# Optimization experiments

Measured on AMD Instinct MI355X. Metric: run time of the kernel, lower is better.

Reference implementation:

```python
import jax, jax.numpy as jnp
import numpy as np

SPACIAL_SCALE = 1.0 / 32
POOLED = 7  # original uses (pooled_height, pooled_height) for both dims


def setup_inputs() -> dict:
    key = jax.random.key(0)
    k_f, k_b, k_x, k_y = jax.random.split(key, 4)
    N, C, H, W = 4, 256, 64, 64
    R = 256
    img = 2047.0  # image-space extent (stride 32 -> 64 feature cells)
    features = jax.random.normal(k_f, (N, C, H, W), dtype=jnp.float32)
    bidx = jax.random.randint(k_b, (R,), 0, N).astype(jnp.float32)
    xs = jnp.sort(jax.random.uniform(k_x, (R, 2), dtype=jnp.float32) * img, axis=1)
    ys = jnp.sort(jax.random.uniform(k_y, (R, 2), dtype=jnp.float32) * img, axis=1)
    # roi = (batch_idx, x_min, y_min, x_max, y_max)
    rois = jnp.stack([bidx, xs[:, 0], ys[:, 0], xs[:, 1], ys[:, 1]], axis=1)
    return {"features": features, "rois": rois}


def _roi_pool(features, rois):
    N, C, H, W = features.shape
    P = POOLED
    neg = -jnp.inf

    bidx = rois[:, 0].astype(jnp.int32)
    # np.round rounds half-to-even; jnp.round matches
    bbox = jnp.round(rois[:, 1:] * SPACIAL_SCALE).astype(jnp.int32)  # [R,4]
    x0 = jnp.clip(bbox[:, 0], 0, W - 1)
    y0 = jnp.clip(bbox[:, 1], 0, H - 1)
    x1 = jnp.clip(bbox[:, 2], 0, W - 1)
    y1 = jnp.clip(bbox[:, 3], 0, H - 1)
    valid = (x0 < x1) & (y0 < y1)  # [R]

    g = features[bidx]  # [R,C,H,W] gathered per-roi feature maps
    Lh = x1 - x0  # rows (H axis) get the x-range -- quirk of the original slice
    Lw = y1 - y0  # cols (W axis) get the y-range

    idx_h = jnp.arange(H)
    idx_w = jnp.arange(W)

    # adaptive_max_pool2d bins: start=floor(i*L/P), end=ceil((i+1)*L/P)
    # Stage 1: reduce W axis into P column bins -> [R,C,H,P]
    cols = []
    for j in range(P):
        s = y0 + (j * Lw) // P
        e = y0 + ((j + 1) * Lw + P - 1) // P
        m = (idx_w[None, :] >= s[:, None]) & (idx_w[None, :] < e[:, None])  # [R,W]
        cols.append(jnp.max(jnp.where(m[:, None, None, :], g, neg), axis=-1))
    s1 = jnp.stack(cols, axis=-1)  # [R,C,H,P]

    # Stage 2: reduce H axis into P row bins -> [R,C,P,P]
    rows = []
    for i in range(P):
        s = x0 + (i * Lh) // P
        e = x0 + ((i + 1) * Lh + P - 1) // P
        m = (idx_h[None, :] >= s[:, None]) & (idx_h[None, :] < e[:, None])  # [R,H]
        rows.append(jnp.max(jnp.where(m[:, None, :, None], s1, neg), axis=2))
    out = jnp.stack(rows, axis=2)  # [R,C,P,P]

    # degenerate rois stay zero (pooled initialized with torch.zeros)
    return jnp.where(valid[:, None, None, None], out, jnp.zeros((), out.dtype))


def reference(features, rois):
    return _roi_pool(features, rois)
```

## Files before the change

### kernel.cpp

```cpp
#include <hip/hip_runtime.h>
#include <math.h>

#define P 7
#define PP (P * P)
#define C 256
#define H 64
#define W 64
#define S (H * W)
#define R_MAX 1024

#define NCP 25
#define RPAD 257

#define TT 64
#define TPAD 65
__global__ __launch_bounds__(256) void transpose_bucket_kernel(
    const float* __restrict__ in, float* __restrict__ outT,
    const float* __restrict__ rois, int* __restrict__ perm, int R)
{
    __shared__ float tile[TT * TPAD];
    const int b   = blockIdx.z;
    const int s0  = blockIdx.x * TT;
    const int c0  = blockIdx.y * TT;
    const int t   = threadIdx.x;
    const int r16 = t >> 4;
    const int m16 = (t & 15) * 4;

    #pragma unroll
    for (int k = 0; k < 4; ++k) {
        const int cl = r16 + 16 * k;
        const float4 v = *(const float4*)(in + (size_t)(b * C + c0 + cl) * S + s0 + m16);
        tile[cl * TPAD + m16 + 0] = v.x;
        tile[cl * TPAD + m16 + 1] = v.y;
        tile[cl * TPAD + m16 + 2] = v.z;
        tile[cl * TPAD + m16 + 3] = v.w;
    }
    __syncthreads();
    #pragma unroll
    for (int k = 0; k < 4; ++k) {
        const int sl = r16 + 16 * k;
        float4 v;
        v.x = tile[(m16 + 0) * TPAD + sl];
        v.y = tile[(m16 + 1) * TPAD + sl];
        v.z = tile[(m16 + 2) * TPAD + sl];
        v.w = tile[(m16 + 3) * TPAD + sl];
        *(float4*)(outT + (size_t)(b * S + s0 + sl) * C + c0 + m16) = v;
    }

    if (blockIdx.x == 0 && blockIdx.y == 0 && blockIdx.z == 0 && R > 0 && R <= R_MAX) {
        __shared__ int bimg[R_MAX];
        for (int i = t; i < R; i += 256)
            bimg[i] = (int)rois[(size_t)i * 5];
        __syncthreads();
        for (int i = t; i < R; i += 256) {
            const int myb = bimg[i];
            int pos = 0;
            for (int k = 0; k < R; ++k) {
                const int bk = bimg[k];
                pos += (bk < myb) || (bk == myb && k < i);
            }
            perm[pos] = i;
        }
    }
}

__global__ __launch_bounds__(128) void roi_pool_cell_kernel(
    const float* __restrict__ ft,
    const float* __restrict__ rois,
    const int*   __restrict__ perm,
    float* __restrict__ ws2)
{
    const int l   = blockIdx.x;
    const int nwg = gridDim.x;
    const int work  = ((nwg & 7) == 0) ? ((l & 7) * (nwg >> 3) + (l >> 3)) : l;
    const int rslot = work / NCP;
    const int cp    = work % NCP;
    const int cell  = 2 * cp + (threadIdx.x >> 6);
    const int q     = threadIdx.x & 63;

    if (cell >= PP) return;

    const int r = perm[rslot];
    const float* roi = rois + (size_t)r * 5;
    const int b = (int)roi[0];
    int x0 = (int)rintf(roi[1] * 0.03125f);
    int y0 = (int)rintf(roi[2] * 0.03125f);
    int x1 = (int)rintf(roi[3] * 0.03125f);
    int y1 = (int)rintf(roi[4] * 0.03125f);
    x0 = min(max(x0, 0), W - 1);
    y0 = min(max(y0, 0), H - 1);
    x1 = min(max(x1, 0), W - 1);
    y1 = min(max(y1, 0), H - 1);

    float4* o = (float4*)(ws2 + ((size_t)rslot * PP + cell) * C) + q;

    if (!((x0 < x1) && (y0 < y1))) {
        *o = make_float4(0.0f, 0.0f, 0.0f, 0.0f);
        return;
    }

    const int Lh = x1 - x0;
    const int Lw = y1 - y0;
    const int i  = cell / P;
    const int j  = cell - P * i;

    const int hs = x0 + (i * Lh) / P;
    const int he = x0 + ((i + 1) * Lh + (P - 1)) / P;
    const int ws = y0 + (j * Lw) / P;
    const int we = y0 + ((j + 1) * Lw + (P - 1)) / P;
    const int bh = he - hs;
    const int bw = we - ws;

    const float* base = ft + (((size_t)b * H + hs) * W + ws) * C + q * 4;

    float mx = -INFINITY, my = -INFINITY, mz = -INFINITY, mw = -INFINITY;
    for (int h = 0; h < bh; h += 2) {
        const int h2 = min(h + 1, bh - 1);
        const float* r0 = base + (size_t)h  * (W * C);
        const float* r1 = base + (size_t)h2 * (W * C);
        for (int w = 0; w < bw; w += 2) {
            const int w2 = min(w + 1, bw - 1);
            const float4 a  = *(const float4*)(r0 + (size_t)w  * C);
            const float4 bb = *(const float4*)(r0 + (size_t)w2 * C);
            const float4 cc = *(const float4*)(r1 + (size_t)w  * C);
            const float4 dd = *(const float4*)(r1 + (size_t)w2 * C);
            mx = fmaxf(fmaxf(fmaxf(mx, a.x), fmaxf(bb.x, cc.x)), dd.x);
            my = fmaxf(fmaxf(fmaxf(my, a.y), fmaxf(bb.y, cc.y)), dd.y);
            mz = fmaxf(fmaxf(fmaxf(mz, a.z), fmaxf(bb.z, cc.z)), dd.z);
            mw = fmaxf(fmaxf(fmaxf(mw, a.w), fmaxf(bb.w, cc.w)), dd.w);
        }
    }

    *o = make_float4(mx, my, mz, mw);
}

__global__ __launch_bounds__(256) void reorder_kernel(
    const float* __restrict__ ws2,
    const int*   __restrict__ perm,
    float* __restrict__ out)
{
    __shared__ float lds[PP * RPAD];
    const int l = blockIdx.x;
    const int R = gridDim.x;
    const int rslot = ((R & 7) == 0) ? ((l & 7) * (R >> 3) + (l >> 3)) : l;
    const int r = perm[rslot];
    const int tid = threadIdx.x;

    const float* src = ws2 + (size_t)rslot * PP * C;
    #pragma unroll
    for (int cell = 0; cell < PP; ++cell)
        lds[cell * RPAD + tid] = src[(size_t)cell * C + tid];

    __syncthreads();

    float* dst = out + (size_t)r * C * PP;
    const int nq = (C * PP) / 4;
    #pragma unroll
    for (int k = 0; k < 13; ++k) {
        const int q = tid + 256 * k;
        if (q < nq) {
            float v[4];
            #pragma unroll
            for (int m = 0; m < 4; ++m) {
                const int idx  = 4 * q + m;
                const int c    = idx / PP;
                const int cell = idx % PP;
                v[m] = lds[cell * RPAD + c];
            }
            *(float4*)(dst + 4 * q) = make_float4(v[0], v[1], v[2], v[3]);
        }
    }
}

__global__ __launch_bounds__(64) void roi_pool_cell_direct_kernel(
    const float* __restrict__ ft, const float* __restrict__ rois,
    float* __restrict__ out)
{
    const int bid = blockIdx.x;
    const int r   = bid / PP;
    const int rem = bid % PP;
    const int i   = rem / P;
    const int j   = rem % P;
    const int c4  = threadIdx.x;

    const float* roi = rois + (size_t)r * 5;
    const int b = (int)roi[0];
    int x0 = (int)rintf(roi[1] * 0.03125f);
    int y0 = (int)rintf(roi[2] * 0.03125f);
    int x1 = (int)rintf(roi[3] * 0.03125f);
    int y1 = (int)rintf(roi[4] * 0.03125f);
    x0 = min(max(x0, 0), W - 1);
    y0 = min(max(y0, 0), H - 1);
    x1 = min(max(x1, 0), W - 1);
    y1 = min(max(y1, 0), H - 1);

    float* o = out + (((size_t)r * C + c4 * 4) * P + i) * P + j;
    if (!((x0 < x1) && (y0 < y1))) {
        o[0] = 0.0f; o[PP] = 0.0f; o[2 * PP] = 0.0f; o[3 * PP] = 0.0f;
        return;
    }
    const int Lh = x1 - x0, Lw = y1 - y0;
    const int hs = x0 + (i * Lh) / P;
    const int he = x0 + ((i + 1) * Lh + (P - 1)) / P;
    const int ws = y0 + (j * Lw) / P;
    const int we = y0 + ((j + 1) * Lw + (P - 1)) / P;
    const int bh = he - hs, bw = we - ws;
    const float* base = ft + (((size_t)b * H + hs) * W + ws) * C + c4 * 4;
    float mx = -INFINITY, my = -INFINITY, mz = -INFINITY, mw = -INFINITY;
    for (int h = 0; h < bh; h += 2) {
        const int h2 = min(h + 1, bh - 1);
        const float* r0 = base + (size_t)h  * (W * C);
        const float* r1 = base + (size_t)h2 * (W * C);
        for (int w = 0; w < bw; w += 2) {
            const int w2 = min(w + 1, bw - 1);
            const float4 a  = *(const float4*)(r0 + (size_t)w  * C);
            const float4 bb = *(const float4*)(r0 + (size_t)w2 * C);
            const float4 cc = *(const float4*)(r1 + (size_t)w  * C);
            const float4 dd = *(const float4*)(r1 + (size_t)w2 * C);
            mx = fmaxf(fmaxf(fmaxf(mx, a.x), fmaxf(bb.x, cc.x)), dd.x);
            my = fmaxf(fmaxf(fmaxf(my, a.y), fmaxf(bb.y, cc.y)), dd.y);
            mz = fmaxf(fmaxf(fmaxf(mz, a.z), fmaxf(bb.z, cc.z)), dd.z);
            mw = fmaxf(fmaxf(fmaxf(mw, a.w), fmaxf(bb.w, cc.w)), dd.w);
        }
    }
    o[0] = mx; o[PP] = my; o[2 * PP] = mz; o[3 * PP] = mw;
}

__global__ __launch_bounds__(256) void roi_pool_naive_kernel(
    const float* __restrict__ features, const float* __restrict__ rois,
    float* __restrict__ out)
{
    const int rb = blockIdx.x;
    const int r = rb / P;
    const int i = rb % P;
    const int c = threadIdx.x;

    const float* roi = rois + (size_t)r * 5;
    const int b = (int)roi[0];
    int x0 = (int)rintf(roi[1] * 0.03125f);
    int y0 = (int)rintf(roi[2] * 0.03125f);
    int x1 = (int)rintf(roi[3] * 0.03125f);
    int y1 = (int)rintf(roi[4] * 0.03125f);
    x0 = min(max(x0, 0), W - 1);
    y0 = min(max(y0, 0), H - 1);
    x1 = min(max(x1, 0), W - 1);
    y1 = min(max(y1, 0), H - 1);

    const bool valid = (x0 < x1) && (y0 < y1);
    float* o = out + (((size_t)r * C + c) * P + i) * P;
    if (!valid) {
        #pragma unroll
        for (int j = 0; j < P; ++j) o[j] = 0.0f;
        return;
    }
    const int Lh = x1 - x0, Lw = y1 - y0;
    const int hs = x0 + (i * Lh) / P;
    const int he = x0 + ((i + 1) * Lh + (P - 1)) / P;
    int ws_[P], we_[P];
    #pragma unroll
    for (int j = 0; j < P; ++j) {
        ws_[j] = y0 + (j * Lw) / P;
        we_[j] = y0 + ((j + 1) * Lw + (P - 1)) / P;
    }
    float acc[P];
    #pragma unroll
    for (int j = 0; j < P; ++j) acc[j] = -INFINITY;
    const float* f = features + (((size_t)b * C + c) * H) * W;
    for (int h = hs; h < he; ++h) {
        const float* row = f + h * W;
        #pragma unroll
        for (int j = 0; j < P; ++j) {
            float m = acc[j];
            for (int w = ws_[j]; w < we_[j]; ++w) m = fmaxf(m, row[w]);
            acc[j] = m;
        }
    }
    #pragma unroll
    for (int j = 0; j < P; ++j) o[j] = acc[j];
}

extern "C" void kernel_launch(void* const* d_in, const int* in_sizes, int n_in,
                              void* d_out, int out_size, void* d_ws, size_t ws_size,
                              hipStream_t stream)
{
    const float* features = (const float*)d_in[0];
    const float* rois     = (const float*)d_in[1];
    float* out = (float*)d_out;

    const int R = in_sizes[1] / 5;
    const int N = in_sizes[0] / (C * S);

    const size_t ft_bytes   = (size_t)N * C * S * sizeof(float);
    const size_t ws2_bytes  = (size_t)R * PP * C * sizeof(float);
    const size_t perm_bytes = (size_t)R * sizeof(int);
    const size_t full_need  = ft_bytes + ws2_bytes + perm_bytes;

    if (ws_size >= full_need && R <= R_MAX) {
        float* ft  = (float*)d_ws;
        float* ws2 = (float*)((char*)d_ws + ft_bytes);
        int*  perm = (int*)((char*)d_ws + ft_bytes + ws2_bytes);

        dim3 tgrid(S / TT, C / TT, N);
        transpose_bucket_kernel<<<tgrid, 256, 0, stream>>>(features, ft, rois, perm, R);
        roi_pool_cell_kernel<<<R * NCP, 128, 0, stream>>>(ft, rois, perm, ws2);
        reorder_kernel<<<R, 256, 0, stream>>>(ws2, perm, out);
    } else if (ws_size >= ft_bytes) {
        float* ft = (float*)d_ws;
        dim3 tgrid(S / TT, C / TT, N);
        transpose_bucket_kernel<<<tgrid, 256, 0, stream>>>(features, ft, rois, (int*)nullptr, 0);
        roi_pool_cell_direct_kernel<<<R * PP, 64, 0, stream>>>(ft, rois, out);
    } else {
        roi_pool_naive_kernel<<<R * P, C, 0, stream>>>(features, rois, out);
    }
}
```

Baseline: 38.18 us.

## Fuse ROI cell pooling and output reorder into one kernel via LDS

Merges the per-cell pooling kernel and the separate reorder kernel into a single kernel. Each 512-thread block handles one ROI and half of the channels, pools all 49 cells into shared memory, then writes the [C,P,P] output layout directly. This removes the intermediate workspace round trip through global memory and one kernel launch. In exchange, loads shrink from float4 to float2 and each wave loops over several cells, which may reduce memory-level parallelism and lengthen the tail for large ROIs.

```diff
diff --git a/kernel.cpp b/kernel.cpp
--- a/kernel.cpp
+++ b/kernel.cpp
@@ -9,8 +9,8 @@
 #define S (H * W)
 #define R_MAX 1024
 
-#define NCP 25
-#define RPAD 257
+#define CHALF 128
+#define LPAD 130
 
 #define TT 64
 #define TPAD 65
@@ -64,21 +64,22 @@
     }
 }
 
-__global__ __launch_bounds__(128) void roi_pool_cell_kernel(
+__global__ __launch_bounds__(512) void roi_pool_out_kernel(
     const float* __restrict__ ft,
     const float* __restrict__ rois,
     const int*   __restrict__ perm,
-    float* __restrict__ ws2)
-{
+    float* __restrict__ out)
+{
+    __shared__ float lds[PP * LPAD];
+
     const int l   = blockIdx.x;
     const int nwg = gridDim.x;
     const int work  = ((nwg & 7) == 0) ? ((l & 7) * (nwg >> 3) + (l >> 3)) : l;
-    const int rslot = work / NCP;
-    const int cp    = work % NCP;
-    const int cell  = 2 * cp + (threadIdx.x >> 6);
-    const int q     = threadIdx.x & 63;
-
-    if (cell >= PP) return;
+    const int rslot = work >> 1;
+    const int half  = work & 1;
+    const int wave  = threadIdx.x >> 6;
+    const int lane  = threadIdx.x & 63;
+    const int c0    = half * CHALF;
 
     const int r = perm[rslot];
     const float* roi = rois + (size_t)r * 5;
@@ -92,82 +93,66 @@
     x1 = min(max(x1, 0), W - 1);
     y1 = min(max(y1, 0), H - 1);
 
-    float4* o = (float4*)(ws2 + ((size_t)rslot * PP + cell) * C) + q;
-
-    if (!((x0 < x1) && (y0 < y1))) {
-        *o = make_float4(0.0f, 0.0f, 0.0f, 0.0f);
-        return;
-    }
-
-    const int Lh = x1 - x0;
-    const int Lw = y1 - y0;
-    const int i  = cell / P;
-    const int j  = cell - P * i;
-
-    const int hs = x0 + (i * Lh) / P;
-    const int he = x0 + ((i + 1) * Lh + (P - 1)) / P;
-    const int ws = y0 + (j * Lw) / P;
-    const int we = y0 + ((j + 1) * Lw + (P - 1)) / P;
-    const int bh = he - hs;
-    const int bw = we - ws;
-
-    const float* base = ft + (((size_t)b * H + hs) * W + ws) * C + q * 4;
-
-    float mx = -INFINITY, my = -INFINITY, mz = -INFINITY, mw = -INFINITY;
-    for (int h = 0; h < bh; h += 2) {
-        const int h2 = min(h + 1, bh - 1);
-        const float* r0 = base + (size_t)h  * (W * C);
-        const float* r1 = base + (size_t)h2 * (W * C);
-        for (int w = 0; w < bw; w += 2) {
-            const int w2 = min(w + 1, bw - 1);
-            const float4 a  = *(const float4*)(r0 + (size_t)w  * C);
-            const float4 bb = *(const float4*)(r0 + (size_t)w2 * C);
-            const float4 cc = *(const float4*)(r1 + (size_t)w  * C);
-            const float4 dd = *(const float4*)(r1 + (size_t)w2 * C);
-            mx = fmaxf(fmaxf(fmaxf(mx, a.x), fmaxf(bb.x, cc.x)), dd.x);
-            my = fmaxf(fmaxf(fmaxf(my, a.y), fmaxf(bb.y, cc.y)), dd.y);
-            mz = fmaxf(fmaxf(fmaxf(mz, a.z), fmaxf(bb.z, cc.z)), dd.z);
-            mw = fmaxf(fmaxf(fmaxf(mw, a.w), fmaxf(bb.w, cc.w)), dd.w);
-        }
-    }
-
-    *o = make_float4(mx, my, mz, mw);
-}
-
-__global__ __launch_bounds__(256) void reorder_kernel(
-    const float* __restrict__ ws2,
-    const int*   __restrict__ perm,
-    float* __restrict__ out)
-{
-    __shared__ float lds[PP * RPAD];
-    const int l = blockIdx.x;
-    const int R = gridDim.x;
-    const int rslot = ((R & 7) == 0) ? ((l & 7) * (R >> 3) + (l >> 3)) : l;
-    const int r = perm[rslot];
-    const int tid = threadIdx.x;
-
-    const float* src = ws2 + (size_t)rslot * PP * C;
-    #pragma unroll
-    for (int cell = 0; cell < PP; ++cell)
-        lds[cell * RPAD + tid] = src[(size_t)cell * C + tid];
+    const bool valid = (x0 < x1) && (y0 < y1);
+
+    if (valid) {
+        const int Lh = x1 - x0;
+        const int Lw = y1 - y0;
+        for (int cell = wave; cell < PP; cell += 8) {
+            const int i = cell / P;
+            const int j = cell - P * i;
+
+            const int hs = x0 + (i * Lh) / P;
+            const int he = x0 + ((i + 1) * Lh + (P - 1)) / P;
+            const int ws = y0 + (j * Lw) / P;
+            const int we = y0 + ((j + 1) * Lw + (P - 1)) / P;
+            const int bh = he - hs;
+            const int bw = we - ws;
+
+            const float* base = ft + (((size_t)b * H + hs) * W + ws) * C + c0 + lane * 2;
+
+            float mx = -INFINITY, my = -INFINITY;
+            for (int h = 0; h < bh; h += 2) {
+                const int h2 = min(h + 1, bh - 1);
+                const float* r0 = base + (size_t)h  * (W * C);
+                const float* r1 = base + (size_t)h2 * (W * C);
+                for (int w = 0; w < bw; w += 2) {
+                    const int w2 = min(w + 1, bw - 1);
+                    const float2 a  = *(const float2*)(r0 + (size_t)w  * C);
+                    const float2 bb = *(const float2*)(r0 + (size_t)w2 * C);
+                    const float2 cc = *(const float2*)(r1 + (size_t)w  * C);
+                    const float2 dd = *(const float2*)(r1 + (size_t)w2 * C);
+                    mx = fmaxf(fmaxf(fmaxf(mx, a.x), fmaxf(bb.x, cc.x)), dd.x);
+                    my = fmaxf(fmaxf(fmaxf(my, a.y), fmaxf(bb.y, cc.y)), dd.y);
+                }
+            }
+            lds[cell * LPAD + lane * 2 + 0] = mx;
+            lds[cell * LPAD + lane * 2 + 1] = my;
+        }
+    } else {
+        for (int cell = wave; cell < PP; cell += 8) {
+            lds[cell * LPAD + lane * 2 + 0] = 0.0f;
+            lds[cell * LPAD + lane * 2 + 1] = 0.0f;
+        }
+    }
 
     __syncthreads();
 
-    float* dst = out + (size_t)r * C * PP;
-    const int nq = (C * PP) / 4;
-    #pragma unroll
-    for (int k = 0; k < 13; ++k) {
-        const int q = tid + 256 * k;
-        if (q < nq) {
+    float* dst = out + ((size_t)r * C + c0) * PP;
+    const int nq = (CHALF * PP) / 4;
+    #pragma unroll
+    for (int k = 0; k < 4; ++k) {
+        const int qf = threadIdx.x + 512 * k;
+        if (qf < nq) {
             float v[4];
             #pragma unroll
             for (int m = 0; m < 4; ++m) {
-                const int idx  = 4 * q + m;
+                const int idx  = 4 * qf + m;
                 const int c    = idx / PP;
-                const int cell = idx % PP;
-                v[m] = lds[cell * RPAD + c];
+                const int cell = idx - PP * c;
+                v[m] = lds[cell * LPAD + c];
             }
-            *(float4*)(dst + 4 * q) = make_float4(v[0], v[1], v[2], v[3]);
+            *(float4*)(dst + 4 * qf) = make_float4(v[0], v[1], v[2], v[3]);
         }
     }
 }
@@ -291,19 +276,16 @@
     const int N = in_sizes[0] / (C * S);
 
     const size_t ft_bytes   = (size_t)N * C * S * sizeof(float);
-    const size_t ws2_bytes  = (size_t)R * PP * C * sizeof(float);
     const size_t perm_bytes = (size_t)R * sizeof(int);
-    const size_t full_need  = ft_bytes + ws2_bytes + perm_bytes;
+    const size_t full_need  = ft_bytes + perm_bytes;
 
     if (ws_size >= full_need && R <= R_MAX) {
         float* ft  = (float*)d_ws;
-        float* ws2 = (float*)((char*)d_ws + ft_bytes);
-        int*  perm = (int*)((char*)d_ws + ft_bytes + ws2_bytes);
+        int*  perm = (int*)((char*)d_ws + ft_bytes);
 
         dim3 tgrid(S / TT, C / TT, N);
         transpose_bucket_kernel<<<tgrid, 256, 0, stream>>>(features, ft, rois, perm, R);
-        roi_pool_cell_kernel<<<R * NCP, 128, 0, stream>>>(ft, rois, perm, ws2);
-        reorder_kernel<<<R, 256, 0, stream>>>(ws2, perm, out);
+        roi_pool_out_kernel<<<R * 2, 512, 0, stream>>>(ft, rois, perm, out);
     } else if (ws_size >= ft_bytes) {
         float* ft = (float*)d_ws;
         dim3 tgrid(S / TT, C / TT, N);
```

New measurement: 54.34 us. +42.3%, slower.
